# Performance work log

Hardware: AMD Instinct MI355X
Metric: run time of the kernel (lower is better)

The kernel has to match this reference:

```python
import jax, jax.numpy as jnp
import numpy as np

FRAMES_IN = 5   # SAMPLING_INPUT_FRAMES = 50 // 10
FRAMES_OUT = 3  # SAMPLING_OUTPUT_FRAMES = 30 // 10
T, N, F, C, H = 512, 60, 2, 64, 512  # trajectories, nodes, features, gcn out, lstm hidden
DIST_THRESH = 10.0
EXIST_THRESH = 0.04


def setup_inputs() -> dict:
    key = jax.random.key(0)
    ks = jax.random.split(key, 24)
    p = {}
    p["feature_input"] = jax.random.normal(ks[0], (FRAMES_IN, T * N, F), jnp.float32)
    p["adj"] = jax.random.randint(ks[1], (FRAMES_IN, T, N, N), 0, 2).astype(jnp.float32)
    p["std"] = jax.random.uniform(ks[2], (F,), jnp.float32)
    p["mean"] = jax.random.normal(ks[3], (F,), jnp.float32)
    # GCNConv params
    p["gcn_W"] = jax.random.normal(ks[4], (F, C), jnp.float32) / np.sqrt(F)
    p["gcn_b"] = jnp.zeros((C,), jnp.float32)
    # LSTM params (PyTorch layout: gates i,f,g,o stacked)
    In = C * N
    s = 1.0 / np.sqrt(H)
    p["W_ih"] = jax.random.uniform(ks[5], (4 * H, In), jnp.float32, -s, s)
    p["W_hh"] = jax.random.uniform(ks[6], (4 * H, H), jnp.float32, -s, s)
    p["b_ih"] = jax.random.uniform(ks[7], (4 * H,), jnp.float32, -s, s)
    p["b_hh"] = jax.random.uniform(ks[8], (4 * H,), jnp.float32, -s, s)
    # MLP: H->512->1028->512->F*N
    def lin(k, fi, fo):
        b = 1.0 / np.sqrt(fi)
        return jax.random.uniform(k, (fi, fo), jnp.float32, -b, b)
    p["W1"] = lin(ks[9], H, 512); p["b1"] = jnp.zeros((512,), jnp.float32)
    p["W2"] = lin(ks[10], 512, 1028); p["b2"] = jnp.zeros((1028,), jnp.float32)
    p["W3"] = lin(ks[11], 1028, 512); p["b3"] = jnp.zeros((512,), jnp.float32)
    p["W4"] = lin(ks[12], 512, F * N); p["b4"] = jnp.zeros((F * N,), jnp.float32)
    return p


def _gcn(x_flat, adjf, gcn_W, gcn_b):
    # x_flat: [T*N, F]; adjf: [T, N, N] block-diagonal graph per trajectory
    x = x_flat.reshape(T, N, F)
    A = adjf + jnp.eye(N, dtype=adjf.dtype)  # PyG GCNConv adds self-loops on top
    deg = A.sum(-1)                            # [T, N]
    norm = jnp.where(deg > 0, jax.lax.rsqrt(deg), 0.0)
    h = x @ gcn_W                              # [T, N, C]
    out = norm[..., None] * jnp.einsum('tij,tjc->tic', A, norm[..., None] * h) + gcn_b
    return out.reshape(T, N * C)


def _lstm(x, h, c, W_ih, W_hh, b_ih, b_hh):
    gates = x @ W_ih.T + b_ih + h @ W_hh.T + b_hh
    i, f, g, o = jnp.split(gates, 4, axis=-1)
    c = jax.nn.sigmoid(f) * c + jax.nn.sigmoid(i) * jnp.tanh(g)
    h = jax.nn.sigmoid(o) * jnp.tanh(c)
    return h, c


def _mlp(h, W1, b1, W2, b2, W3, b3, W4, b4):
    h = jax.nn.relu(h @ W1 + b1)
    h = jax.nn.relu(h @ W2 + b2)
    h = jax.nn.relu(h @ W3 + b3)
    return h @ W4 + b4  # [T, F*N]


def _find_adj(pred, std, mean):
    # radius-graph construction (denormalized coords, block per trajectory)
    x = jax.lax.stop_gradient(pred * std + mean).reshape(T, N, F)
    exist = (x[..., 0] > EXIST_THRESH) & (x[..., 1] > EXIST_THRESH)  # [T, N]
    diff = x[:, :, None, :2] - x[:, None, :, :2]
    dist = jnp.sqrt(jnp.sum(diff * diff, -1))                        # [T, N, N]
    eye = jnp.eye(N, dtype=bool)
    conn = ((dist > 0) & (dist < DIST_THRESH)) | eye
    adj = exist[:, :, None] & exist[:, None, :] & conn
    return adj.astype(pred.dtype)


def reference(feature_input, adj, std, mean, gcn_W, gcn_b, W_ih, W_hh, b_ih, b_hh,
              W1, b1, W2, b2, W3, b3, W4, b4):
    h = jnp.zeros((T, H), feature_input.dtype)
    c = jnp.zeros((T, H), feature_input.dtype)
    enc = [feature_input[0]]
    for i in range(FRAMES_IN - 1):  # break at last frame in original
        g = _gcn(feature_input[i], adj[i], gcn_W, gcn_b)
        h, c = _lstm(g, h, c, W_ih, W_hh, b_ih, b_hh)
        pred = _mlp(h, W1, b1, W2, b2, W3, b3, W4, b4).reshape(T * N, F)
        enc.append(pred)
    cur_x, cur_adj = feature_input[FRAMES_IN - 1], adj[FRAMES_IN - 1]
    dec = []
    for _ in range(FRAMES_OUT):
        g = _gcn(cur_x, cur_adj, gcn_W, gcn_b)
        h, c = _lstm(g, h, c, W_ih, W_hh, b_ih, b_hh)
        pred = _mlp(h, W1, b1, W2, b2, W3, b3, W4, b4).reshape(T * N, F)
        dec.append(pred)
        cur_x = pred
        cur_adj = _find_adj(pred, std, mean)
    return jnp.stack(enc), jnp.stack(dec)
```

## Files before the change

### kernel.cpp

```cpp
#include <hip/hip_runtime.h>

#define T_ 512
#define N_ 60
#define F_ 2
#define C_ 64
#define H_ 512
#define IN_ 3840
#define FOURH 2048
#define PRED_SZ 61440
#define ADJ_SZ 1843200
#define K2_ 128
#define LDSK 40
#define HSLOT 262144

typedef __attribute__((ext_vector_type(8))) short bf8;
typedef __attribute__((ext_vector_type(4))) float f4;

__device__ __forceinline__ unsigned short f2bf(float f)
{
    unsigned int u = __float_as_uint(f);
    u = (u + 0x7FFFu + ((u >> 16) & 1u)) >> 16;
    return (unsigned short)u;
}

__global__ void prep_init_k(const float* Whh, const float* W1, const float* W2,
                            const float* W3, const float* W4, const float* feat,
                            unsigned short* Whh_bf, unsigned short* W1_bf,
                            unsigned short* W2_bf, unsigned short* W3_bf,
                            unsigned short* W4_bf,
                            unsigned short* hAll, float* c, float* out)
{
    long i = (long)blockIdx.x * 256 + threadIdx.x;
    if (i < 1048576) { Whh_bf[i] = f2bf(Whh[i]); return; }
    i -= 1048576;
    if (i < 262144) { W1_bf[i] = f2bf(W1[i]); return; }
    i -= 262144;
    if (i < 526336) { W2_bf[i] = f2bf(W2[i]); return; }
    i -= 526336;
    if (i < 526336) { W3_bf[i] = f2bf(W3[i]); return; }
    i -= 526336;
    if (i < 61440) { W4_bf[i] = f2bf(W4[i]); return; }
    i -= 61440;
    hAll[i] = 0;
    c[i] = 0.0f;
    if (i < PRED_SZ) out[i] = feat[i];
}

__global__ __launch_bounds__(256) void wih2_k(
    const float* Wih, const float* W, const float* b,
    const float* bih, const float* bhh,
    unsigned short* Wih2_bf, float* biasAll)
{
    __shared__ float row[IN_];
    __shared__ float wc[2][64];
    __shared__ float bb[64];
    __shared__ float red[256];

    int o = blockIdx.x;
    int tid = threadIdx.x;

    if (tid < 128) wc[tid >> 6][tid & 63] = W[tid];
    if (tid < 64) bb[tid] = b[tid];
    for (int k = tid; k < IN_; k += 256) row[k] = Wih[(long)o * IN_ + k];
    __syncthreads();

    if (tid < 128) {
        float s = 0.0f;
        if (tid < 120) {
            int n = tid >> 1;
            int f = tid & 1;
            for (int c2 = 0; c2 < 64; ++c2) s += row[n * 64 + c2] * wc[f][c2];
        }
        Wih2_bf[(long)o * K2_ + tid] = f2bf(s);
    }

    float sb = 0.0f;
    for (int k = tid; k < IN_; k += 256) sb += row[k] * bb[k & 63];
    red[tid] = sb;
    __syncthreads();
    for (int s = 128; s > 0; s >>= 1) {
        if (tid < s) red[tid] += red[tid + s];
        __syncthreads();
    }
    if (tid == 0) biasAll[o] = bih[o] + bhh[o] + red[0];
}

__global__ __launch_bounds__(128) void gcn_enc_y(
    const float* x, const float* adj, unsigned short* Y)
{
    __shared__ float sA[N_][N_];
    __shared__ float sx[N_][2];
    __shared__ float snorm[N_];

    int frame = blockIdx.x >> 9;
    int t = blockIdx.x & 511;
    const float* xf = x + (long)frame * PRED_SZ + (long)t * 120;
    const float* af = adj + (long)frame * ADJ_SZ + (long)t * 3600;
    int tid = threadIdx.x;

    for (int l = tid; l < N_ * N_; l += 128) {
        int i = l / N_;
        int j = l - i * N_;
        float a = af[l];
        if (i == j) a += 1.0f;
        sA[i][j] = a;
    }
    if (tid < 120) sx[tid >> 1][tid & 1] = xf[tid];
    __syncthreads();

    if (tid < N_) {
        float d = 0.0f;
        for (int j = 0; j < N_; ++j) d += sA[tid][j];
        snorm[tid] = (d > 0.0f) ? rsqrtf(d) : 0.0f;
    }
    __syncthreads();

    if (tid < 128) {
        float y = 0.0f;
        if (tid < 120) {
            int n = tid >> 1;
            int f = tid & 1;
            float s = 0.0f;
            for (int j = 0; j < N_; ++j) s += sA[n][j] * snorm[j] * sx[j][f];
            y = snorm[n] * s;
        }
        Y[(long)blockIdx.x * K2_ + tid] = f2bf(y);
    }
}

__global__ __launch_bounds__(128) void gcn_dec_y(
    const float* pred, const float* stdv, const float* meanv, unsigned short* Y)
{
    __shared__ float sA[N_][N_];
    __shared__ float sx[N_][2];
    __shared__ float dx0[N_];
    __shared__ float dx1[N_];
    __shared__ int sex[N_];
    __shared__ float snorm[N_];

    int t = blockIdx.x;
    int tid = threadIdx.x;
    const float* pr = pred + (long)t * 120;

    if (tid < 120) sx[tid >> 1][tid & 1] = pr[tid];
    if (tid < N_) {
        float vx = pr[tid * 2 + 0] * stdv[0] + meanv[0];
        float vy = pr[tid * 2 + 1] * stdv[1] + meanv[1];
        dx0[tid] = vx;
        dx1[tid] = vy;
        sex[tid] = (vx > 0.04f) && (vy > 0.04f);
    }
    __syncthreads();

    for (int l = tid; l < N_ * N_; l += 128) {
        int i = l / N_;
        int j = l - i * N_;
        float ddx = dx0[i] - dx0[j];
        float ddy = dx1[i] - dx1[j];
        float d = sqrtf(ddx * ddx + ddy * ddy);
        int conn = ((d > 0.0f) && (d < 10.0f)) || (i == j);
        float a = (sex[i] && sex[j] && conn) ? 1.0f : 0.0f;
        if (i == j) a += 1.0f;
        sA[i][j] = a;
    }
    __syncthreads();

    if (tid < N_) {
        float d = 0.0f;
        for (int j = 0; j < N_; ++j) d += sA[tid][j];
        snorm[tid] = (d > 0.0f) ? rsqrtf(d) : 0.0f;
    }
    __syncthreads();

    if (tid < 128) {
        float y = 0.0f;
        if (tid < 120) {
            int n = tid >> 1;
            int f = tid & 1;
            float s = 0.0f;
            for (int j = 0; j < N_; ++j) s += sA[n][j] * snorm[j] * sx[j][f];
            y = snorm[n] * s;
        }
        Y[(long)t * K2_ + tid] = f2bf(y);
    }
}

__global__ __launch_bounds__(256) void mlp_gemm(
    const unsigned short* Abf, const unsigned short* Bb,
    const float* bias1, float* Cf, unsigned short* Cbf,
    int M, int Nc, int K, int mode)
{
    __shared__ unsigned short As[2][32 * LDSK];
    __shared__ unsigned short Bs[2][32 * LDSK];

    int tid = threadIdx.x;
    int wave = tid >> 6;
    int wt = wave >> 1, wj = wave & 1;
    int lane = tid & 63;
    int quad = lane >> 4;
    int l16 = lane & 15;
    int row0 = blockIdx.y * 32;
    int col0 = blockIdx.x * 32;

    f4 acc = {0.f, 0.f, 0.f, 0.f};
    const ushort4 zu = make_ushort4(0, 0, 0, 0);

    int sr = tid >> 3;
    int sko = (tid & 7) * 4;

    auto loadA = [&](int k0, ushort4& v) {
        int gm = row0 + sr, gk = k0 + sko;
        v = zu;
        if (gm < M && gk + 4 <= K) v = *(const ushort4*)&Abf[(long)gm * K + gk];
    };
    auto loadB = [&](int k0, ushort4& v) {
        int gk = k0 + sr;
        int gn0 = col0 + sko;
        v = zu;
        if (gk < K) {
            if (gn0 + 4 <= Nc) {
                v = *(const ushort4*)&Bb[(long)gk * Nc + gn0];
            } else {
                unsigned short tmp[4] = {0, 0, 0, 0};
                for (int i = 0; i < 4; ++i)
                    if (gn0 + i < Nc) tmp[i] = Bb[(long)gk * Nc + gn0 + i];
                v = make_ushort4(tmp[0], tmp[1], tmp[2], tmp[3]);
            }
        }
    };

    int niter = (K + 31) / 32;
    ushort4 a0, b0, a1 = zu, b1 = zu, a2 = zu, b2 = zu;
    loadA(0, a0);
    loadB(0, b0);
    if (niter > 1) { loadA(32, a1); loadB(32, b1); }

    for (int it = 0; it < niter; ++it) {
        if (it + 2 < niter) {
            loadA((it + 2) * 32, a2);
            loadB((it + 2) * 32, b2);
        }
        int bf = it & 1;
        *(ushort4*)&As[bf][sr * LDSK + sko] = a0;
        Bs[bf][(sko + 0) * LDSK + sr] = b0.x;
        Bs[bf][(sko + 1) * LDSK + sr] = b0.y;
        Bs[bf][(sko + 2) * LDSK + sr] = b0.z;
        Bs[bf][(sko + 3) * LDSK + sr] = b0.w;
        __syncthreads();

        bf8 fa = *(const bf8*)&As[bf][(wt * 16 + l16) * LDSK + quad * 8];
        bf8 fb = *(const bf8*)&Bs[bf][(wj * 16 + l16) * LDSK + quad * 8];
        acc = __builtin_amdgcn_mfma_f32_16x16x32_bf16(fa, fb, acc, 0, 0, 0);

        a0 = a1; a1 = a2; b0 = b1; b1 = b2;
    }

    int gn = col0 + wj * 16 + l16;
    if (gn < Nc) {
        float bsv = bias1[gn];
        #pragma unroll
        for (int r = 0; r < 4; ++r) {
            int gm = row0 + wt * 16 + quad * 4 + r;
            if (gm >= M) continue;
            float v = acc[r] + bsv;
            long idx = (long)gm * Nc + gn;
            if (mode == 2) {
                if (v < 0.0f) v = 0.0f;
                Cbf[idx] = f2bf(v);
            } else {
                Cf[idx] = v;
            }
        }
    }
}

__global__ __launch_bounds__(256) void mlp_w1b(
    const unsigned short* hAll, const unsigned short* Bb,
    const float* bias1, unsigned short* Cbf)
{
    __shared__ unsigned short As[2][32 * LDSK];
    __shared__ unsigned short Bs[2][32 * LDSK];

    int tid = threadIdx.x;
    int wave = tid >> 6;
    int wt = wave >> 1, wj = wave & 1;
    int lane = tid & 63;
    int quad = lane >> 4;
    int l16 = lane & 15;
    int row0 = blockIdx.y * 32;
    int col0 = blockIdx.x * 32;

    f4 acc = {0.f, 0.f, 0.f, 0.f};
    int sr = tid >> 3;
    int sko = (tid & 7) * 4;

    int gr = row0 + sr;
    int sidx = gr >> 9;
    int slot = (sidx < 4) ? (sidx + 1) : 7;
    const unsigned short* arow = hAll + (long)slot * HSLOT + (long)(gr & 511) * H_;

    auto loadA = [&](int k0, ushort4& v) {
        v = *(const ushort4*)&arow[k0 + sko];
    };
    auto loadB = [&](int k0, ushort4& v) {
        v = *(const ushort4*)&Bb[(long)(k0 + sr) * 512 + col0 + sko];
    };

    ushort4 a0, b0, a1, b1, a2 = make_ushort4(0,0,0,0), b2 = a2;
    loadA(0, a0); loadB(0, b0);
    loadA(32, a1); loadB(32, b1);

    for (int it = 0; it < 16; ++it) {
        if (it + 2 < 16) { loadA((it + 2) * 32, a2); loadB((it + 2) * 32, b2); }
        int bf = it & 1;
        *(ushort4*)&As[bf][sr * LDSK + sko] = a0;
        Bs[bf][(sko + 0) * LDSK + sr] = b0.x;
        Bs[bf][(sko + 1) * LDSK + sr] = b0.y;
        Bs[bf][(sko + 2) * LDSK + sr] = b0.z;
        Bs[bf][(sko + 3) * LDSK + sr] = b0.w;
        __syncthreads();

        bf8 fa = *(const bf8*)&As[bf][(wt * 16 + l16) * LDSK + quad * 8];
        bf8 fb = *(const bf8*)&Bs[bf][(wj * 16 + l16) * LDSK + quad * 8];
        acc = __builtin_amdgcn_mfma_f32_16x16x32_bf16(fa, fb, acc, 0, 0, 0);

        a0 = a1; a1 = a2; b0 = b1; b1 = b2;
    }

    int gn = col0 + wj * 16 + l16;
    float bsv = bias1[gn];
    #pragma unroll
    for (int r = 0; r < 4; ++r) {
        int gm = row0 + wt * 16 + quad * 4 + r;
        float v = acc[r] + bsv;
        if (v < 0.0f) v = 0.0f;
        Cbf[(long)gm * 512 + gn] = f2bf(v);
    }
}

__global__ __launch_bounds__(256) void mlp_w4b(
    const unsigned short* Abf, const unsigned short* Bb,
    const float* bias1, float* out)
{
    __shared__ unsigned short As[2][32 * LDSK];
    __shared__ unsigned short Bs[2][32 * LDSK];

    int tid = threadIdx.x;
    int wave = tid >> 6;
    int wt = wave >> 1, wj = wave & 1;
    int lane = tid & 63;
    int quad = lane >> 4;
    int l16 = lane & 15;
    int row0 = blockIdx.y * 32;
    int col0 = blockIdx.x * 32;

    f4 acc = {0.f, 0.f, 0.f, 0.f};
    const ushort4 zu = make_ushort4(0, 0, 0, 0);
    int sr = tid >> 3;
    int sko = (tid & 7) * 4;

    auto loadA = [&](int k0, ushort4& v) {
        v = *(const ushort4*)&Abf[(long)(row0 + sr) * 512 + k0 + sko];
    };
    auto loadB = [&](int k0, ushort4& v) {
        int gn0 = col0 + sko;
        v = zu;
        if (gn0 + 4 <= 120) {
            v = *(const ushort4*)&Bb[(long)(k0 + sr) * 120 + gn0];
        } else {
            unsigned short tmp[4] = {0, 0, 0, 0};
            for (int i = 0; i < 4; ++i)
                if (gn0 + i < 120) tmp[i] = Bb[(long)(k0 + sr) * 120 + gn0 + i];
            v = make_ushort4(tmp[0], tmp[1], tmp[2], tmp[3]);
        }
    };

    ushort4 a0, b0, a1, b1, a2 = zu, b2 = zu;
    loadA(0, a0); loadB(0, b0);
    loadA(32, a1); loadB(32, b1);

    for (int it = 0; it < 16; ++it) {
        if (it + 2 < 16) { loadA((it + 2) * 32, a2); loadB((it + 2) * 32, b2); }
        int bf = it & 1;
        *(ushort4*)&As[bf][sr * LDSK + sko] = a0;
        Bs[bf][(sko + 0) * LDSK + sr] = b0.x;
        Bs[bf][(sko + 1) * LDSK + sr] = b0.y;
        Bs[bf][(sko + 2) * LDSK + sr] = b0.z;
        Bs[bf][(sko + 3) * LDSK + sr] = b0.w;
        __syncthreads();

        bf8 fa = *(const bf8*)&As[bf][(wt * 16 + l16) * LDSK + quad * 8];
        bf8 fb = *(const bf8*)&Bs[bf][(wj * 16 + l16) * LDSK + quad * 8];
        acc = __builtin_amdgcn_mfma_f32_16x16x32_bf16(fa, fb, acc, 0, 0, 0);

        a0 = a1; a1 = a2; b0 = b1; b1 = b2;
    }

    int gn = col0 + wj * 16 + l16;
    if (gn < 120) {
        float bsv = bias1[gn];
        #pragma unroll
        for (int r = 0; r < 4; ++r) {
            int gm = row0 + wt * 16 + quad * 4 + r;
            int sidx = gm >> 9;
            int frame = (sidx < 4) ? (sidx + 1) : 7;
            out[(long)frame * PRED_SZ + (long)(gm & 511) * 120 + gn] = acc[r] + bsv;
        }
    }
}

__global__ __launch_bounds__(256) void whh_lstm_k(
    const unsigned short* hprev, const unsigned short* Whh_bf,
    const unsigned short* Yf, const unsigned short* Wih2_bf,
    const float* biasAll, float* c, unsigned short* hnew)
{
    __shared__ unsigned short As[2][32 * LDSK];
    __shared__ unsigned short Bs[2][128 * LDSK];

    int tid = threadIdx.x;
    int wave = tid >> 6;
    int wt = wave >> 1, wj = wave & 1;
    int lane = tid & 63;
    int quad = lane >> 4;
    int l16 = lane & 15;
    int j0 = blockIdx.x * 32;
    int row0 = blockIdx.y * 32;

    int sr = tid >> 3;
    int sko = (tid & 7) * 4;
    int br = tid >> 1;
    int bko = (tid & 1) * 16;
    long brow = (long)((br >> 5) * H_ + j0 + (br & 31));
    long bb_w = brow * H_;
    long bb_y = brow * K2_;
    long ar_h = (long)(row0 + sr) * H_;
    long ar_y = (long)(row0 + sr) * K2_;

    f4 acc[4];
    #pragma unroll
    for (int g = 0; g < 4; ++g) acc[g] = f4{0.f, 0.f, 0.f, 0.f};

    auto loadT = [&](int it, ushort4& a, uint4& q0, uint4& q1) {
        if (it < 4) {
            int k = it * 32;
            a  = *(const ushort4*)&Yf[ar_y + k + sko];
            q0 = *(const uint4*)&Wih2_bf[bb_y + k + bko];
            q1 = *(const uint4*)&Wih2_bf[bb_y + k + bko + 8];
        } else {
            int k = (it - 4) * 32;
            a  = *(const ushort4*)&hprev[ar_h + k + sko];
            q0 = *(const uint4*)&Whh_bf[bb_w + k + bko];
            q1 = *(const uint4*)&Whh_bf[bb_w + k + bko + 8];
        }
    };

    ushort4 a0, a1, a2 = make_ushort4(0, 0, 0, 0);
    uint4 q00, q01, q10, q11, q20 = uint4{0,0,0,0}, q21 = uint4{0,0,0,0};
    loadT(0, a0, q00, q01);
    loadT(1, a1, q10, q11);

    for (int it = 0; it < 20; ++it) {
        if (it + 2 < 20) loadT(it + 2, a2, q20, q21);
        int bf = it & 1;
        *(ushort4*)&As[bf][sr * LDSK + sko] = a0;
        *(uint4*)&Bs[bf][br * LDSK + bko]     = q00;
        *(uint4*)&Bs[bf][br * LDSK + bko + 8] = q01;
        __syncthreads();

        bf8 fa = *(const bf8*)&As[bf][(wt * 16 + l16) * LDSK + quad * 8];
        #pragma unroll
        for (int g = 0; g < 4; ++g) {
            bf8 fb = *(const bf8*)&Bs[bf][(g * 32 + wj * 16 + l16) * LDSK + quad * 8];
            acc[g] = __builtin_amdgcn_mfma_f32_16x16x32_bf16(fa, fb, acc[g], 0, 0, 0);
        }

        a0 = a1; a1 = a2;
        q00 = q10; q01 = q11; q10 = q20; q11 = q21;
    }

    int j = j0 + wj * 16 + l16;
    float b_i = biasAll[j];
    float b_f = biasAll[512 + j];
    float b_g = biasAll[1024 + j];
    float b_o = biasAll[1536 + j];
    #pragma unroll
    for (int r = 0; r < 4; ++r) {
        int t = row0 + wt * 16 + quad * 4 + r;
        float gi = acc[0][r] + b_i;
        float gf = acc[1][r] + b_f;
        float gg = acc[2][r] + b_g;
        float go = acc[3][r] + b_o;
        float ig = 1.0f / (1.0f + expf(-gi));
        float fg = 1.0f / (1.0f + expf(-gf));
        float g2 = tanhf(gg);
        float og = 1.0f / (1.0f + expf(-go));
        long ci = (long)t * H_ + j;
        float cn = fg * c[ci] + ig * g2;
        c[ci] = cn;
        hnew[ci] = f2bf(og * tanhf(cn));
    }
}

extern "C" void kernel_launch(void* const* d_in, const int* in_sizes, int n_in,
                              void* d_out, int out_size, void* d_ws, size_t ws_size,
                              hipStream_t stream)
{
    const float* feat  = (const float*)d_in[0];
    const float* adjin = (const float*)d_in[1];
    const float* stdv  = (const float*)d_in[2];
    const float* meanv = (const float*)d_in[3];
    const float* gcnW  = (const float*)d_in[4];
    const float* gcnb  = (const float*)d_in[5];
    const float* Wih   = (const float*)d_in[6];
    const float* Whh   = (const float*)d_in[7];
    const float* bih   = (const float*)d_in[8];
    const float* bhh   = (const float*)d_in[9];
    const float* W1    = (const float*)d_in[10];
    const float* b1    = (const float*)d_in[11];
    const float* W2    = (const float*)d_in[12];
    const float* b2    = (const float*)d_in[13];
    const float* W3    = (const float*)d_in[14];
    const float* b3    = (const float*)d_in[15];
    const float* W4    = (const float*)d_in[16];
    const float* b4    = (const float*)d_in[17];
    float* out = (float*)d_out;

    float* c       = (float*)d_ws;
    float* biasAll = c + 262144;
    unsigned short* Y       = (unsigned short*)(biasAll + 2048);
    unsigned short* hAll    = Y + 5 * 65536;
    unsigned short* m1      = hAll + 8 * HSLOT;
    unsigned short* m2      = m1 + 1310720;
    unsigned short* m3      = m2 + 2631680;
    unsigned short* Whh_bf  = m3 + 1310720;
    unsigned short* W1_bf   = Whh_bf + 1048576;
    unsigned short* W2_bf   = W1_bf + 262144;
    unsigned short* W3_bf   = W2_bf + 526336;
    unsigned short* W4_bf   = W3_bf + 526336;
    unsigned short* Wih2_bf = W4_bf + 61440;

    prep_init_k<<<10496, 256, 0, stream>>>(Whh, W1, W2, W3, W4, feat,
                                           Whh_bf, W1_bf, W2_bf, W3_bf, W4_bf,
                                           hAll, c, out);
    wih2_k<<<FOURH, 256, 0, stream>>>(Wih, gcnW, gcnb, bih, bhh, Wih2_bf, biasAll);
    gcn_enc_y<<<5 * T_, 128, 0, stream>>>(feat, adjin, Y);

    for (int s = 0; s < 5; ++s)
        whh_lstm_k<<<dim3(16, 16), 256, 0, stream>>>(hAll + (long)s * HSLOT,
                                                     Whh_bf, Y + (long)s * 65536,
                                                     Wih2_bf, biasAll, c,
                                                     hAll + (long)(s + 1) * HSLOT);

    for (int s = 4; s <= 5; ++s) {
        const unsigned short* hs = hAll + (long)(s + 1) * HSLOT;
        mlp_gemm<<<dim3(16, 16), 256, 0, stream>>>(hs, W1_bf, b1,
                                                   (float*)0, m1, T_, 512, 512, 2);
        mlp_gemm<<<dim3(33, 16), 256, 0, stream>>>(m1, W2_bf, b2,
                                                   (float*)0, m2, T_, 1028, 512, 2);
        mlp_gemm<<<dim3(16, 16), 256, 0, stream>>>(m2, W3_bf, b3,
                                                   (float*)0, m3, T_, 512, 1028, 2);
        mlp_gemm<<<dim3(4, 16), 256, 0, stream>>>(m3, W4_bf, b4,
                                                  out + (long)(s + 1) * PRED_SZ,
                                                  (unsigned short*)0, T_, 120, 512, 3);
        gcn_dec_y<<<T_, 128, 0, stream>>>(out + (long)(s + 1) * PRED_SZ,
                                          stdv, meanv, Y);
        whh_lstm_k<<<dim3(16, 16), 256, 0, stream>>>(hAll + (long)(s + 1) * HSLOT,
                                                     Whh_bf, Y, Wih2_bf, biasAll, c,
                                                     hAll + (long)(s + 2) * HSLOT);
    }

    mlp_w1b<<<dim3(16, 80), 256, 0, stream>>>(hAll, W1_bf, b1, m1);
    mlp_gemm<<<dim3(33, 80), 256, 0, stream>>>(m1, W2_bf, b2,
                                               (float*)0, m2, 2560, 1028, 512, 2);
    mlp_gemm<<<dim3(16, 80), 256, 0, stream>>>(m2, W3_bf, b3,
                                               (float*)0, m3, 2560, 512, 1028, 2);
    mlp_w4b<<<dim3(4, 80), 256, 0, stream>>>(m3, W4_bf, b4, out);
}
```

Before: 374.4 us.

## Merge prep kernels, retile LSTM step and batched MLP GEMMs to 64x64

Folds the three setup kernels (weight bf16 conversion, Wih×GCN weight folding, encoder GCN aggregation) into one launch, which cuts launch overhead and lets the pieces overlap. The LSTM step kernel now uses 16-row tiles across twice as many blocks. It skips the W_hh GEMM on the first step, where h is zero, and computes the gate nonlinearities from a shared-memory staging of the gate accumulators. The batched MLP layers W1–W3 move to a 64x64 tile GEMM with four MFMAs per wave, which increases operand reuse. A separate decoder Y buffer is added.

```diff
diff --git a/kernel.cpp b/kernel.cpp
--- a/kernel.cpp
+++ b/kernel.cpp
@@ -23,108 +23,113 @@
     return (unsigned short)u;
 }
 
-__global__ void prep_init_k(const float* Whh, const float* W1, const float* W2,
-                            const float* W3, const float* W4, const float* feat,
-                            unsigned short* Whh_bf, unsigned short* W1_bf,
-                            unsigned short* W2_bf, unsigned short* W3_bf,
-                            unsigned short* W4_bf,
-                            unsigned short* hAll, float* c, float* out)
-{
-    long i = (long)blockIdx.x * 256 + threadIdx.x;
-    if (i < 1048576) { Whh_bf[i] = f2bf(Whh[i]); return; }
-    i -= 1048576;
-    if (i < 262144) { W1_bf[i] = f2bf(W1[i]); return; }
-    i -= 262144;
-    if (i < 526336) { W2_bf[i] = f2bf(W2[i]); return; }
-    i -= 526336;
-    if (i < 526336) { W3_bf[i] = f2bf(W3[i]); return; }
-    i -= 526336;
-    if (i < 61440) { W4_bf[i] = f2bf(W4[i]); return; }
-    i -= 61440;
-    hAll[i] = 0;
-    c[i] = 0.0f;
-    if (i < PRED_SZ) out[i] = feat[i];
-}
-
-__global__ __launch_bounds__(256) void wih2_k(
-    const float* Wih, const float* W, const float* b,
-    const float* bih, const float* bhh,
-    unsigned short* Wih2_bf, float* biasAll)
-{
-    __shared__ float row[IN_];
-    __shared__ float wc[2][64];
-    __shared__ float bb[64];
-    __shared__ float red[256];
-
-    int o = blockIdx.x;
+__global__ __launch_bounds__(256) void prep_all_k(
+    const float* Whh, const float* W1, const float* W2,
+    const float* W3, const float* W4, const float* feat,
+    const float* Wih, const float* gcnW, const float* gcnb,
+    const float* bih, const float* bhh, const float* adj,
+    unsigned short* Whh_bf, unsigned short* W1_bf, unsigned short* W2_bf,
+    unsigned short* W3_bf, unsigned short* W4_bf,
+    unsigned short* hAll, float* c, float* out,
+    unsigned short* Wih2_bf, float* biasAll, unsigned short* Y)
+{
+    __shared__ __align__(16) unsigned char smem[30720];
+    int bid = blockIdx.x;
     int tid = threadIdx.x;
 
-    if (tid < 128) wc[tid >> 6][tid & 63] = W[tid];
-    if (tid < 64) bb[tid] = b[tid];
-    for (int k = tid; k < IN_; k += 256) row[k] = Wih[(long)o * IN_ + k];
-    __syncthreads();
-
-    if (tid < 128) {
-        float s = 0.0f;
-        if (tid < 120) {
-            int n = tid >> 1;
-            int f = tid & 1;
-            for (int c2 = 0; c2 < 64; ++c2) s += row[n * 64 + c2] * wc[f][c2];
-        }
-        Wih2_bf[(long)o * K2_ + tid] = f2bf(s);
-    }
-
-    float sb = 0.0f;
-    for (int k = tid; k < IN_; k += 256) sb += row[k] * bb[k & 63];
-    red[tid] = sb;
-    __syncthreads();
-    for (int s = 128; s > 0; s >>= 1) {
-        if (tid < s) red[tid] += red[tid + s];
-        __syncthreads();
-    }
-    if (tid == 0) biasAll[o] = bih[o] + bhh[o] + red[0];
-}
-
-__global__ __launch_bounds__(128) void gcn_enc_y(
-    const float* x, const float* adj, unsigned short* Y)
-{
-    __shared__ float sA[N_][N_];
-    __shared__ float sx[N_][2];
-    __shared__ float snorm[N_];
-
-    int frame = blockIdx.x >> 9;
-    int t = blockIdx.x & 511;
-    const float* xf = x + (long)frame * PRED_SZ + (long)t * 120;
-    const float* af = adj + (long)frame * ADJ_SZ + (long)t * 3600;
-    int tid = threadIdx.x;
-
-    for (int l = tid; l < N_ * N_; l += 128) {
-        int i = l / N_;
-        int j = l - i * N_;
-        float a = af[l];
-        if (i == j) a += 1.0f;
-        sA[i][j] = a;
-    }
-    if (tid < 120) sx[tid >> 1][tid & 1] = xf[tid];
-    __syncthreads();
-
-    if (tid < N_) {
-        float d = 0.0f;
-        for (int j = 0; j < N_; ++j) d += sA[tid][j];
-        snorm[tid] = (d > 0.0f) ? rsqrtf(d) : 0.0f;
-    }
-    __syncthreads();
-
-    if (tid < 128) {
+    if (bid < 10496) {
+        long i = (long)bid * 256 + tid;
+        if (i < 1048576) { Whh_bf[i] = f2bf(Whh[i]); return; }
+        i -= 1048576;
+        if (i < 262144) { W1_bf[i] = f2bf(W1[i]); return; }
+        i -= 262144;
+        if (i < 526336) { W2_bf[i] = f2bf(W2[i]); return; }
+        i -= 526336;
+        if (i < 526336) { W3_bf[i] = f2bf(W3[i]); return; }
+        i -= 526336;
+        if (i < 61440) { W4_bf[i] = f2bf(W4[i]); return; }
+        i -= 61440;
+        hAll[i] = 0;
+        c[i] = 0.0f;
+        if (i < PRED_SZ) out[i] = feat[i];
+        return;
+    }
+
+    if (bid < 12544) {
+        int o = bid - 10496;
+        float* row = (float*)smem;
+        float* wc  = row + IN_;
+        float* bb  = wc + 128;
+        float* red = bb + 64;
+
+        if (tid < 128) wc[tid] = gcnW[tid];
+        if (tid < 64) bb[tid] = gcnb[tid];
+        for (int k = tid; k < IN_; k += 256) row[k] = Wih[(long)o * IN_ + k];
+        __syncthreads();
+
+        if (tid < 128) {
+            float s = 0.0f;
+            if (tid < 120) {
+                int n = tid >> 1;
+                int f = tid & 1;
+                for (int c2 = 0; c2 < 64; ++c2) s += row[n * 64 + c2] * wc[f * 64 + c2];
+            }
+            Wih2_bf[(long)o * K2_ + tid] = f2bf(s);
+        }
+
+        float sb = 0.0f;
+        for (int k = tid; k < IN_; k += 256) sb += row[k] * bb[k & 63];
+        red[tid] = sb;
+        __syncthreads();
+        for (int s = 128; s > 0; s >>= 1) {
+            if (tid < s) red[tid] += red[tid + s];
+            __syncthreads();
+        }
+        if (tid == 0) biasAll[o] = bih[o] + bhh[o] + red[0];
+        return;
+    }
+
+    {
+        int gid = bid - 12544;
+        int half = tid >> 7;
+        int lt = tid & 127;
+        int tg = gid * 2 + half;
+        int frame = tg >> 9;
+        int t = tg & 511;
+
+        float* sA    = (float*)(smem + half * 15120);
+        float* sx    = sA + 3600;
+        float* snorm = sx + 120;
+
+        const float* xf = feat + (long)frame * PRED_SZ + (long)t * 120;
+        const float* af = adj + (long)frame * ADJ_SZ + (long)t * 3600;
+
+        for (int l = lt; l < N_ * N_; l += 128) {
+            int i = l / N_;
+            int j = l - i * N_;
+            float a = af[l];
+            if (i == j) a += 1.0f;
+            sA[l] = a;
+        }
+        if (lt < 120) sx[lt] = xf[lt];
+        __syncthreads();
+
+        if (lt < N_) {
+            float d = 0.0f;
+            for (int j = 0; j < N_; ++j) d += sA[lt * N_ + j];
+            snorm[lt] = (d > 0.0f) ? rsqrtf(d) : 0.0f;
+        }
+        __syncthreads();
+
         float y = 0.0f;
-        if (tid < 120) {
-            int n = tid >> 1;
-            int f = tid & 1;
+        if (lt < 120) {
+            int n = lt >> 1;
+            int f = lt & 1;
             float s = 0.0f;
-            for (int j = 0; j < N_; ++j) s += sA[n][j] * snorm[j] * sx[j][f];
+            for (int j = 0; j < N_; ++j) s += sA[n * N_ + j] * snorm[j] * sx[j * 2 + f];
             y = snorm[n] * s;
         }
-        Y[(long)blockIdx.x * K2_ + tid] = f2bf(y);
+        Y[(long)tg * K2_ + lt] = f2bf(y);
     }
 }
 
@@ -204,7 +209,6 @@
 
     f4 acc = {0.f, 0.f, 0.f, 0.f};
     const ushort4 zu = make_ushort4(0, 0, 0, 0);
-
     int sr = tid >> 3;
     int sko = (tid & 7) * 4;
 
@@ -274,67 +278,134 @@
     }
 }
 
-__global__ __launch_bounds__(256) void mlp_w1b(
-    const unsigned short* hAll, const unsigned short* Bb,
-    const float* bias1, unsigned short* Cbf)
-{
-    __shared__ unsigned short As[2][32 * LDSK];
-    __shared__ unsigned short Bs[2][32 * LDSK];
+__global__ __launch_bounds__(256) void b64_k(
+    const unsigned short* Abf, const unsigned short* hAll, int indirect,
+    const unsigned short* Bb, const float* bias1, unsigned short* Cbf,
+    int M, int Nc, int K)
+{
+    __shared__ unsigned short As[2][64 * LDSK];
+    __shared__ unsigned short Bs[2][64 * LDSK];
 
     int tid = threadIdx.x;
     int wave = tid >> 6;
-    int wt = wave >> 1, wj = wave & 1;
     int lane = tid & 63;
     int quad = lane >> 4;
     int l16 = lane & 15;
-    int row0 = blockIdx.y * 32;
-    int col0 = blockIdx.x * 32;
-
-    f4 acc = {0.f, 0.f, 0.f, 0.f};
-    int sr = tid >> 3;
-    int sko = (tid & 7) * 4;
-
-    int gr = row0 + sr;
-    int sidx = gr >> 9;
-    int slot = (sidx < 4) ? (sidx + 1) : 7;
-    const unsigned short* arow = hAll + (long)slot * HSLOT + (long)(gr & 511) * H_;
-
-    auto loadA = [&](int k0, ushort4& v) {
-        v = *(const ushort4*)&arow[k0 + sko];
+    int wr = (wave >> 1) * 32;
+    int wc = (wave & 1) * 32;
+    int row0 = blockIdx.y * 64;
+    int col0 = blockIdx.x * 64;
+
+    f4 acc00 = {0.f,0.f,0.f,0.f}, acc01 = {0.f,0.f,0.f,0.f};
+    f4 acc10 = {0.f,0.f,0.f,0.f}, acc11 = {0.f,0.f,0.f,0.f};
+    const ushort4 zu = make_ushort4(0, 0, 0, 0);
+
+    int ar = tid >> 2;
+    int ako = (tid & 3) * 8;
+    int bkk = tid >> 3;
+    int bnp = (tid & 7) * 8;
+
+    int gr = row0 + ar;
+    const unsigned short* arow;
+    if (indirect) {
+        int sidx = gr >> 9;
+        int slot = (sidx < 4) ? (sidx + 1) : 7;
+        arow = hAll + (long)slot * HSLOT + (long)(gr & 511) * K;
+    } else {
+        arow = Abf + (long)gr * K;
+    }
+
+    auto loadA = [&](int k0, ushort4& v0, ushort4& v1) {
+        int gk = k0 + ako;
+        v0 = zu; v1 = zu;
+        if (gk + 4 <= K) v0 = *(const ushort4*)&arow[gk];
+        if (gk + 8 <= K) v1 = *(const ushort4*)&arow[gk + 4];
     };
-    auto loadB = [&](int k0, ushort4& v) {
-        v = *(const ushort4*)&Bb[(long)(k0 + sr) * 512 + col0 + sko];
+    auto loadB = [&](int k0, ushort4& v0, ushort4& v1) {
+        int gk = k0 + bkk;
+        int gn0 = col0 + bnp;
+        v0 = zu; v1 = zu;
+        if (gk < K) {
+            if (gn0 + 4 <= Nc) {
+                v0 = *(const ushort4*)&Bb[(long)gk * Nc + gn0];
+            } else {
+                unsigned short t0[4] = {0,0,0,0};
+                for (int i = 0; i < 4; ++i)
+                    if (gn0 + i < Nc) t0[i] = Bb[(long)gk * Nc + gn0 + i];
+                v0 = make_ushort4(t0[0], t0[1], t0[2], t0[3]);
+            }
+            if (gn0 + 8 <= Nc) {
+                v1 = *(const ushort4*)&Bb[(long)gk * Nc + gn0 + 4];
+            } else {
+                unsigned short t1[4] = {0,0,0,0};
+                for (int i = 0; i < 4; ++i)
+                    if (gn0 + 4 + i < Nc) t1[i] = Bb[(long)gk * Nc + gn0 + 4 + i];
+                v1 = make_ushort4(t1[0], t1[1], t1[2], t1[3]);
+            }
+        }
     };
 
-    ushort4 a0, b0, a1, b1, a2 = make_ushort4(0,0,0,0), b2 = a2;
-    loadA(0, a0); loadB(0, b0);
-    loadA(32, a1); loadB(32, b1);
-
-    for (int it = 0; it < 16; ++it) {
-        if (it + 2 < 16) { loadA((it + 2) * 32, a2); loadB((it + 2) * 32, b2); }
+    int niter = (K + 31) / 32;
+    ushort4 a00, a01, b00, b01;
+    ushort4 a10 = zu, a11 = zu, b10 = zu, b11 = zu;
+    ushort4 a20 = zu, a21 = zu, b20 = zu, b21 = zu;
+    loadA(0, a00, a01);
+    loadB(0, b00, b01);
+    if (niter > 1) { loadA(32, a10, a11); loadB(32, b10, b11); }
+
+    for (int it = 0; it < niter; ++it) {
+        if (it + 2 < niter) {
+            loadA((it + 2) * 32, a20, a21);
+            loadB((it + 2) * 32, b20, b21);
+        }
         int bf = it & 1;
-        *(ushort4*)&As[bf][sr * LDSK + sko] = a0;
-        Bs[bf][(sko + 0) * LDSK + sr] = b0.x;
-        Bs[bf][(sko + 1) * LDSK + sr] = b0.y;
-        Bs[bf][(sko + 2) * LDSK + sr] = b0.z;
-        Bs[bf][(sko + 3) * LDSK + sr] = b0.w;
-        __syncthreads();
-
-        bf8 fa = *(const bf8*)&As[bf][(wt * 16 + l16) * LDSK + quad * 8];
-        bf8 fb = *(const bf8*)&Bs[bf][(wj * 16 + l16) * LDSK + quad * 8];
-        acc = __builtin_amdgcn_mfma_f32_16x16x32_bf16(fa, fb, acc, 0, 0, 0);
-
-        a0 = a1; a1 = a2; b0 = b1; b1 = b2;
-    }
-
-    int gn = col0 + wj * 16 + l16;
-    float bsv = bias1[gn];
+        *(ushort4*)&As[bf][ar * LDSK + ako]     = a00;
+        *(ushort4*)&As[bf][ar * LDSK + ako + 4] = a01;
+        Bs[bf][(bnp + 0) * LDSK + bkk] = b00.x;
+        Bs[bf][(bnp + 1) * LDSK + bkk] = b00.y;
+        Bs[bf][(bnp + 2) * LDSK + bkk] = b00.z;
+        Bs[bf][(bnp + 3) * LDSK + bkk] = b00.w;
+        Bs[bf][(bnp + 4) * LDSK + bkk] = b01.x;
+        Bs[bf][(bnp + 5) * LDSK + bkk] = b01.y;
+        Bs[bf][(bnp + 6) * LDSK + bkk] = b01.z;
+        Bs[bf][(bnp + 7) * LDSK + bkk] = b01.w;
+        __syncthreads();
+
+        bf8 fa0 = *(const bf8*)&As[bf][(wr + l16) * LDSK + quad * 8];
+        bf8 fa1 = *(const bf8*)&As[bf][(wr + 16 + l16) * LDSK + quad * 8];
+        bf8 fb0 = *(const bf8*)&Bs[bf][(wc + l16) * LDSK + quad * 8];
+        bf8 fb1 = *(const bf8*)&Bs[bf][(wc + 16 + l16) * LDSK + quad * 8];
+
+        acc00 = __builtin_amdgcn_mfma_f32_16x16x32_bf16(fa0, fb0, acc00, 0, 0, 0);
+        acc01 = __builtin_amdgcn_mfma_f32_16x16x32_bf16(fa0, fb1, acc01, 0, 0, 0);
+        acc10 = __builtin_amdgcn_mfma_f32_16x16x32_bf16(fa1, fb0, acc10, 0, 0, 0);
+        acc11 = __builtin_amdgcn_mfma_f32_16x16x32_bf16(fa1, fb1, acc11, 0, 0, 0);
+        __syncthreads();
+
+        a00 = a10; a01 = a11; a10 = a20; a11 = a21;
+        b00 = b10; b01 = b11; b10 = b20; b11 = b21;
+    }
+
     #pragma unroll
-    for (int r = 0; r < 4; ++r) {
-        int gm = row0 + wt * 16 + quad * 4 + r;
-        float v = acc[r] + bsv;
-        if (v < 0.0f) v = 0.0f;
-        Cbf[(long)gm * 512 + gn] = f2bf(v);
+    for (int mi = 0; mi < 2; ++mi) {
+        #pragma unroll
+        for (int ni = 0; ni < 2; ++ni) {
+            int gn = col0 + wc + ni * 16 + l16;
+            if (gn >= Nc) continue;
+            float bsv = bias1[gn];
+            #pragma unroll
+            for (int r = 0; r < 4; ++r) {
+                int gm = row0 + wr + mi * 16 + quad * 4 + r;
+                float v;
+                if (mi == 0 && ni == 0) v = acc00[r];
+                else if (mi == 0)       v = acc01[r];
+                else if (ni == 0)       v = acc10[r];
+                else                    v = acc11[r];
+                v += bsv;
+                if (v < 0.0f) v = 0.0f;
+                Cbf[(long)gm * Nc + gn] = f2bf(v);
+            }
+        }
     }
 }
 
@@ -409,92 +480,103 @@
     }
 }
 
-__global__ __launch_bounds__(256) void whh_lstm_k(
+__global__ __launch_bounds__(256) void whh_lstm2_k(
     const unsigned short* hprev, const unsigned short* Whh_bf,
     const unsigned short* Yf, const unsigned short* Wih2_bf,
-    const float* biasAll, float* c, unsigned short* hnew)
-{
-    __shared__ unsigned short As[2][32 * LDSK];
-    __shared__ unsigned short Bs[2][128 * LDSK];
+    const float* biasAll, float* c, unsigned short* hnew, int withH)
+{
+    __shared__ __align__(16) union {
+        struct {
+            unsigned short A[2][16 * LDSK];
+            unsigned short B[2][128 * LDSK];
+        } s;
+        float g[4][16][32];
+    } sm;
 
     int tid = threadIdx.x;
-    int wave = tid >> 6;
-    int wt = wave >> 1, wj = wave & 1;
+    int g = tid >> 6;
     int lane = tid & 63;
     int quad = lane >> 4;
     int l16 = lane & 15;
     int j0 = blockIdx.x * 32;
-    int row0 = blockIdx.y * 32;
-
-    int sr = tid >> 3;
-    int sko = (tid & 7) * 4;
+    int row0 = blockIdx.y * 16;
+
+    int asr = tid >> 3;
+    int ako = (tid & 7) * 4;
     int br = tid >> 1;
     int bko = (tid & 1) * 16;
     long brow = (long)((br >> 5) * H_ + j0 + (br & 31));
     long bb_w = brow * H_;
     long bb_y = brow * K2_;
-    long ar_h = (long)(row0 + sr) * H_;
-    long ar_y = (long)(row0 + sr) * K2_;
-
-    f4 acc[4];
-    #pragma unroll
-    for (int g = 0; g < 4; ++g) acc[g] = f4{0.f, 0.f, 0.f, 0.f};
+    long ar_h = (long)(row0 + asr) * H_;
+    long ar_y = (long)(row0 + asr) * K2_;
+
+    f4 acc[2];
+    acc[0] = f4{0.f, 0.f, 0.f, 0.f};
+    acc[1] = f4{0.f, 0.f, 0.f, 0.f};
+
+    int niter = withH ? 20 : 4;
 
     auto loadT = [&](int it, ushort4& a, uint4& q0, uint4& q1) {
         if (it < 4) {
             int k = it * 32;
-            a  = *(const ushort4*)&Yf[ar_y + k + sko];
+            if (tid < 128) a = *(const ushort4*)&Yf[ar_y + k + ako];
             q0 = *(const uint4*)&Wih2_bf[bb_y + k + bko];
             q1 = *(const uint4*)&Wih2_bf[bb_y + k + bko + 8];
         } else {
             int k = (it - 4) * 32;
-            a  = *(const ushort4*)&hprev[ar_h + k + sko];
+            if (tid < 128) a = *(const ushort4*)&hprev[ar_h + k + ako];
             q0 = *(const uint4*)&Whh_bf[bb_w + k + bko];
             q1 = *(const uint4*)&Whh_bf[bb_w + k + bko + 8];
         }
     };
 
-    ushort4 a0, a1, a2 = make_ushort4(0, 0, 0, 0);
+    ushort4 a0 = make_ushort4(0,0,0,0), a1 = a0, a2 = a0;
     uint4 q00, q01, q10, q11, q20 = uint4{0,0,0,0}, q21 = uint4{0,0,0,0};
     loadT(0, a0, q00, q01);
     loadT(1, a1, q10, q11);
 
-    for (int it = 0; it < 20; ++it) {
-        if (it + 2 < 20) loadT(it + 2, a2, q20, q21);
+    for (int it = 0; it < niter; ++it) {
+        if (it + 2 < niter) loadT(it + 2, a2, q20, q21);
         int bf = it & 1;
-        *(ushort4*)&As[bf][sr * LDSK + sko] = a0;
-        *(uint4*)&Bs[bf][br * LDSK + bko]     = q00;
-        *(uint4*)&Bs[bf][br * LDSK + bko + 8] = q01;
-        __syncthreads();
-
-        bf8 fa = *(const bf8*)&As[bf][(wt * 16 + l16) * LDSK + quad * 8];
+        if (tid < 128) *(ushort4*)&sm.s.A[bf][asr * LDSK + ako] = a0;
+        *(uint4*)&sm.s.B[bf][br * LDSK + bko]     = q00;
+        *(uint4*)&sm.s.B[bf][br * LDSK + bko + 8] = q01;
+        __syncthreads();
+
+        bf8 fa = *(const bf8*)&sm.s.A[bf][l16 * LDSK + quad * 8];
         #pragma unroll
-        for (int g = 0; g < 4; ++g) {
-            bf8 fb = *(const bf8*)&Bs[bf][(g * 32 + wj * 16 + l16) * LDSK + quad * 8];
-            acc[g] = __builtin_amdgcn_mfma_f32_16x16x32_bf16(fa, fb, acc[g], 0, 0, 0);
+        for (int jh = 0; jh < 2; ++jh) {
+            bf8 fb = *(const bf8*)&sm.s.B[bf][(g * 32 + jh * 16 + l16) * LDSK + quad * 8];
+            acc[jh] = __builtin_amdgcn_mfma_f32_16x16x32_bf16(fa, fb, acc[jh], 0, 0, 0);
         }
 
         a0 = a1; a1 = a2;
         q00 = q10; q01 = q11; q10 = q20; q11 = q21;
     }
 
-    int j = j0 + wj * 16 + l16;
-    float b_i = biasAll[j];
-    float b_f = biasAll[512 + j];
-    float b_g = biasAll[1024 + j];
-    float b_o = biasAll[1536 + j];
+    __syncthreads();
     #pragma unroll
-    for (int r = 0; r < 4; ++r) {
-        int t = row0 + wt * 16 + quad * 4 + r;
-        float gi = acc[0][r] + b_i;
-        float gf = acc[1][r] + b_f;
-        float gg = acc[2][r] + b_g;
-        float go = acc[3][r] + b_o;
+    for (int jh = 0; jh < 2; ++jh)
+        #pragma unroll
+        for (int r = 0; r < 4; ++r)
+            sm.g[g][quad * 4 + r][jh * 16 + l16] = acc[jh][r];
+    __syncthreads();
+
+    for (int cell = tid; cell < 512; cell += 256) {
+        int tloc = cell >> 5;
+        int j = cell & 31;
+        int t = row0 + tloc;
+        int jg = j0 + j;
+        float gi = sm.g[0][tloc][j] + biasAll[jg];
+        float gf = sm.g[1][tloc][j] + biasAll[512 + jg];
+        float gg = sm.g[2][tloc][j] + biasAll[1024 + jg];
+        float go = sm.g[3][tloc][j] + biasAll[1536 + jg];
         float ig = 1.0f / (1.0f + expf(-gi));
         float fg = 1.0f / (1.0f + expf(-gf));
         float g2 = tanhf(gg);
         float og = 1.0f / (1.0f + expf(-go));
-        long ci = (long)t * H_ + j;
+        long ci = (long)t * H_ + jg;
         float cn = fg * c[ci] + ig * g2;
         c[ci] = cn;
         hnew[ci] = f2bf(og * tanhf(cn));
@@ -528,7 +610,8 @@
     float* c       = (float*)d_ws;
     float* biasAll = c + 262144;
     unsigned short* Y       = (unsigned short*)(biasAll + 2048);
-    unsigned short* hAll    = Y + 5 * 65536;
+    unsigned short* Ydec    = Y + 5 * 65536;
+    unsigned short* hAll    = Y + 6 * 65536;
     unsigned short* m1      = hAll + 8 * HSLOT;
     unsigned short* m2      = m1 + 1310720;
     unsigned short* m3      = m2 + 2631680;
@@ -539,17 +622,17 @@
     unsigned short* W4_bf   = W3_bf + 526336;
     unsigned short* Wih2_bf = W4_bf + 61440;
 
-    prep_init_k<<<10496, 256, 0, stream>>>(Whh, W1, W2, W3, W4, feat,
-                                           Whh_bf, W1_bf, W2_bf, W3_bf, W4_bf,
-                                           hAll, c, out);
-    wih2_k<<<FOURH, 256, 0, stream>>>(Wih, gcnW, gcnb, bih, bhh, Wih2_bf, biasAll);
-    gcn_enc_y<<<5 * T_, 128, 0, stream>>>(feat, adjin, Y);
+    prep_all_k<<<13824, 256, 0, stream>>>(Whh, W1, W2, W3, W4, feat,
+                                          Wih, gcnW, gcnb, bih, bhh, adjin,
+                                          Whh_bf, W1_bf, W2_bf, W3_bf, W4_bf,
+                                          hAll, c, out, Wih2_bf, biasAll, Y);
 
     for (int s = 0; s < 5; ++s)
-        whh_lstm_k<<<dim3(16, 16), 256, 0, stream>>>(hAll + (long)s * HSLOT,
-                                                     Whh_bf, Y + (long)s * 65536,
-                                                     Wih2_bf, biasAll, c,
-                                                     hAll + (long)(s + 1) * HSLOT);
+        whh_lstm2_k<<<dim3(16, 32), 256, 0, stream>>>(hAll + (long)s * HSLOT,
+                                                      Whh_bf, Y + (long)s * 65536,
+                                                      Wih2_bf, biasAll, c,
+                                                      hAll + (long)(s + 1) * HSLOT,
+                                                      s > 0);
 
     for (int s = 4; s <= 5; ++s) {
         const unsigned short* hs = hAll + (long)(s + 1) * HSLOT;
@@ -563,16 +646,17 @@
                                                   out + (long)(s + 1) * PRED_SZ,
                                                   (unsigned short*)0, T_, 120, 512, 3);
         gcn_dec_y<<<T_, 128, 0, stream>>>(out + (long)(s + 1) * PRED_SZ,
-                                          stdv, meanv, Y);
-        whh_lstm_k<<<dim3(16, 16), 256, 0, stream>>>(hAll + (long)(s + 1) * HSLOT,
-                                                     Whh_bf, Y, Wih2_bf, biasAll, c,
-                                                     hAll + (long)(s + 2) * HSLOT);
-    }
-
-    mlp_w1b<<<dim3(16, 80), 256, 0, stream>>>(hAll, W1_bf, b1, m1);
-    mlp_gemm<<<dim3(33, 80), 256, 0, stream>>>(m1, W2_bf, b2,
-                                               (float*)0, m2, 2560, 1028, 512, 2);
-    mlp_gemm<<<dim3(16, 80), 256, 0, stream>>>(m2, W3_bf, b3,
-                                               (float*)0, m3, 2560, 512, 1028, 2);
+                                          stdv, meanv, Ydec);
+        whh_lstm2_k<<<dim3(16, 32), 256, 0, stream>>>(hAll + (long)(s + 1) * HSLOT,
+                                                      Whh_bf, Ydec, Wih2_bf, biasAll, c,
+                                                      hAll + (long)(s + 2) * HSLOT, 1);
+    }
+
+    b64_k<<<dim3(8, 40), 256, 0, stream>>>((const unsigned short*)0, hAll, 1,
+                                           W1_bf, b1, m1, 2560, 512, 512);
+    b64_k<<<dim3(17, 40), 256, 0, stream>>>(m1, (const unsigned short*)0, 0,
+                                            W2_bf, b2, m2, 2560, 1028, 512);
+    b64_k<<<dim3(8, 40), 256, 0, stream>>>(m2, (const unsigned short*)0, 0,
+                                           W3_bf, b3, m3, 2560, 512, 1028);
     mlp_w4b<<<dim3(4, 80), 256, 0, stream>>>(m3, W4_bf, b4, out);
 }
```

Result: slower. 402.4 us (+7.5%).
